# Kernel optimization log

Hardware: AMD Instinct MI355X
Metric: run time of the kernel (lower is better)

## Reference

```python
import jax, jax.numpy as jnp
import numpy as np

NUM_MEM, MEM_DIM, INP_DIM, N = 4096, 512, 1024, 32768

def setup_inputs() -> dict:
    key = jax.random.key(0)
    ks = jax.random.split(key, 6)
    s = 1.0 / np.sqrt(MEM_DIM)
    return {
        "k": jax.random.normal(ks[0], (N, INP_DIM), dtype=jnp.float32),
        "mem": jax.random.normal(ks[1], (NUM_MEM, MEM_DIM), dtype=jnp.float32),
        "fk_w": jax.random.uniform(ks[2], (INP_DIM, MEM_DIM), jnp.float32, -s, s),
        "fk_b": jax.random.uniform(ks[3], (INP_DIM,), jnp.float32, -s, s),
        "fv_w": jax.random.uniform(ks[4], (INP_DIM, MEM_DIM), jnp.float32, -s, s),
        "fv_b": jax.random.uniform(ks[5], (INP_DIM,), jnp.float32, -s, s),
    }

def reference(k, mem, fk_w, fk_b, fv_w, fv_b):
    # key/value derivation from the memory bank: [num_mem, inp_dim]
    key = jax.nn.softmax(mem @ fk_w.T + fk_b, axis=-1)
    val = jax.nn.relu(mem @ fv_w.T + fv_b)
    # attention read: [n, num_mem]
    att = jax.nn.softmax(k @ key.T, axis=-1)
    # output: [n, inp_dim]
    return att @ val
```

## Files before the change

### kernel.cpp

```cpp
#include <hip/hip_runtime.h>
#include <stdint.h>

typedef unsigned short u16;
typedef short s16x8 __attribute__((ext_vector_type(8)));
typedef float f32x4 __attribute__((ext_vector_type(4)));

__device__ __forceinline__ u16 f2bf(float f) {
    union { float f; uint32_t i; } v; v.f = f;
    return (u16)((v.i + 0x7FFFu + ((v.i >> 16) & 1u)) >> 16);
}

__global__ void __launch_bounds__(256) cvt_f32_bf16(
    const float* __restrict__ src, u16* __restrict__ dst, int n4)
{
    int i = blockIdx.x * 256 + threadIdx.x;
    if (i >= n4) return;
    float4 f = ((const float4*)src)[i];
    ushort4 o;
    o.x = f2bf(f.x); o.y = f2bf(f.y); o.z = f2bf(f.z); o.w = f2bf(f.w);
    ((ushort4*)dst)[i] = o;
}

#define ASYNC_LD16(gp, lp)                                                       \
    __builtin_amdgcn_global_load_lds(                                            \
        (const __attribute__((address_space(1))) uint32_t*)(gp),                 \
        (__attribute__((address_space(3))) uint32_t*)(lp), 16, 0, 0)

template <int MODE>
__global__ void __launch_bounds__(256) gemm_bt(
    const u16* __restrict__ A, const u16* __restrict__ B, int K, int N,
    u16* __restrict__ C, float* __restrict__ Cf,
    const float* __restrict__ bias,
    const float* __restrict__ sv, float* __restrict__ sum_out)
{
    __shared__ __align__(16) u16 As[128 * 32];
    __shared__ __align__(16) u16 Bs[128 * 32];

    const int tid  = threadIdx.x;
    const int lane = tid & 63;
    const int wave = tid >> 6;
    const int wx = wave & 1, wy = wave >> 1;
    const int lr = lane & 15, lq = lane >> 4;
    const int m0 = blockIdx.y * 128, n0 = blockIdx.x * 128;

    f32x4 acc[4][4] = {};

    const int srow = tid >> 2;
    const int scol = (tid & 3) * 8;
    const u16* gA = A + (size_t)(m0 + srow) * K + scol;
    const u16* gB = B + (size_t)(n0 + srow) * K + scol;
    const size_t rstep = (size_t)64 * K;
    u16* lA0 = &As[wave * 512];
    u16* lA1 = &As[2048 + wave * 512];
    u16* lB0 = &Bs[wave * 512];
    u16* lB1 = &Bs[2048 + wave * 512];

    const u16* pa = &As[(wy * 64 + lr) * 32 + lq * 8];
    const u16* pb = &Bs[(wx * 64 + lr) * 32 + lq * 8];

    for (int k0 = 0; k0 < K; k0 += 32) {
        ASYNC_LD16(gA + k0, lA0);
        ASYNC_LD16(gA + k0 + rstep, lA1);
        ASYNC_LD16(gB + k0, lB0);
        ASYNC_LD16(gB + k0 + rstep, lB1);
        __syncthreads();
        s16x8 af[4], bfr[4];
#pragma unroll
        for (int i = 0; i < 4; ++i) {
            af[i]  = *(const s16x8*)(pa + i * 512);
            bfr[i] = *(const s16x8*)(pb + i * 512);
        }
#pragma unroll
        for (int mi = 0; mi < 4; ++mi)
#pragma unroll
            for (int ni = 0; ni < 4; ++ni)
                acc[mi][ni] = __builtin_amdgcn_mfma_f32_16x16x32_bf16(
                    af[mi], bfr[ni], acc[mi][ni], 0, 0, 0);
        __syncthreads();
    }

    const int rowB = m0 + wy * 64 + lq * 4;
    const int colB = n0 + wx * 64 + lr;

    if constexpr (MODE == 0) {
        float bcol[4];
#pragma unroll
        for (int ni = 0; ni < 4; ++ni) bcol[ni] = bias[colB + ni * 16];
#pragma unroll
        for (int mi = 0; mi < 4; ++mi)
#pragma unroll
            for (int r = 0; r < 4; ++r) {
                const int gm = rowB + mi * 16 + r;
                float s = 0.f;
#pragma unroll
                for (int ni = 0; ni < 4; ++ni) {
                    float e = __expf(acc[mi][ni][r] + bcol[ni]);
                    C[(size_t)gm * N + (colB + ni * 16)] = f2bf(e);
                    s += e;
                }
                s += __shfl_xor(s, 1);
                s += __shfl_xor(s, 2);
                s += __shfl_xor(s, 4);
                s += __shfl_xor(s, 8);
                if (lr == 0) atomicAdd(&sum_out[gm], s);
            }
    } else {
#pragma unroll
        for (int mi = 0; mi < 4; ++mi)
#pragma unroll
            for (int r = 0; r < 4; ++r) {
                const int gm = rowB + mi * 16 + r;
                const float b = bias[gm];
#pragma unroll
                for (int ni = 0; ni < 4; ++ni) {
                    float c = acc[mi][ni][r] + b;
                    C[(size_t)gm * N + (colB + ni * 16)] = f2bf(c > 0.f ? c : 0.f);
                }
            }
    }
}

template <int MODE>
__global__ void __launch_bounds__(512, 2) gemm256_bt(
    const u16* __restrict__ A, const u16* __restrict__ B, int K, int N,
    u16* __restrict__ C, float* __restrict__ Cf,
    const float* __restrict__ sv, float* __restrict__ sum_out, int nbx)
{
    __shared__ __align__(16) u16 lds[4 * 16384];

    const int tid  = threadIdx.x;
    const int lane = tid & 63;
    const int wave = tid >> 6;
    const int wr = wave >> 2;
    const int wc = wave & 3;
    const int fr = lane & 15;
    const int lq = lane >> 4;

    const int nwg = gridDim.x;
    const int swz = ((int)blockIdx.x & 7) * (nwg >> 3) + ((int)blockIdx.x >> 3);
    const int bx = swz % nbx, by = swz / nbx;
    const int m0 = by * 256, n0 = bx * 256;

    const int r0 = tid >> 2;
    const int r1 = r0 + 128;
    const int gch = (tid & 3) ^ ((r0 >> 1) & 3);
    const u16* gA0 = A + (size_t)(m0 + r0) * K + gch * 8;
    const u16* gA1 = A + (size_t)(m0 + r1) * K + gch * 8;
    const u16* gB0 = B + (size_t)(n0 + r0) * K + gch * 8;
    const u16* gB1 = B + (size_t)(n0 + r1) * K + gch * 8;

#define STG_A(bf_, kt_) do {                                                  \
        ASYNC_LD16(gA0 + (kt_) * 32, lds + (bf_) * 16384 + wave * 512);       \
        ASYNC_LD16(gA1 + (kt_) * 32, lds + (bf_) * 16384 + 4096 + wave * 512);\
    } while (0)
#define STG_B(bf_, kt_) do {                                                  \
        ASYNC_LD16(gB0 + (kt_) * 32, lds + (bf_) * 16384 + 8192 + wave * 512);\
        ASYNC_LD16(gB1 + (kt_) * 32, lds + (bf_) * 16384 + 12288 + wave * 512);\
    } while (0)

    const int rch = lq ^ ((fr >> 1) & 3);
    const int offA0 = (wr * 128 + fr) * 32 + rch * 8;
    const int offB0 = (wc * 64 + fr) * 32 + rch * 8;

    f32x4 acc[8][4] = {};
    const int NT = K >> 5;

    STG_A(0, 0); STG_B(0, 0);
    STG_A(1, 1); STG_B(1, 1);
    STG_A(2, 2); STG_B(2, 2);
    asm volatile("s_waitcnt vmcnt(8)" ::: "memory");
    __builtin_amdgcn_s_barrier();

    for (int c = 0; c < NT; ++c) {
        const u16* sA = lds + (c & 3) * 16384;
        const u16* sB = sA + 8192;
        s16x8 a0[4], b0[4], a1[4];
#pragma unroll
        for (int i = 0; i < 4; ++i) a0[i] = *(const s16x8*)(sA + offA0 + i * 512);
#pragma unroll
        for (int i = 0; i < 4; ++i) b0[i] = *(const s16x8*)(sB + offB0 + i * 512);
        if (c + 3 < NT) STG_A((c + 3) & 3, c + 3);
        __builtin_amdgcn_s_barrier();
        asm volatile("s_waitcnt lgkmcnt(0)" ::: "memory");
        __builtin_amdgcn_s_setprio(1);
#pragma unroll
        for (int mi = 0; mi < 4; ++mi)
#pragma unroll
            for (int ni = 0; ni < 4; ++ni)
                acc[mi][ni] = __builtin_amdgcn_mfma_f32_16x16x32_bf16(
                    a0[mi], b0[ni], acc[mi][ni], 0, 0, 0);
        __builtin_amdgcn_s_setprio(0);
        __builtin_amdgcn_s_barrier();
#pragma unroll
        for (int i = 0; i < 4; ++i) a1[i] = *(const s16x8*)(sA + offA0 + (i + 4) * 512);
        if (c + 3 < NT) STG_B((c + 3) & 3, c + 3);
        __builtin_amdgcn_s_barrier();
        asm volatile("s_waitcnt lgkmcnt(0)" ::: "memory");
        __builtin_amdgcn_s_setprio(1);
#pragma unroll
        for (int mi = 0; mi < 4; ++mi)
#pragma unroll
            for (int ni = 0; ni < 4; ++ni)
                acc[mi + 4][ni] = __builtin_amdgcn_mfma_f32_16x16x32_bf16(
                    a1[mi], b0[ni], acc[mi + 4][ni], 0, 0, 0);
        __builtin_amdgcn_s_setprio(0);
        asm volatile("s_waitcnt vmcnt(8)" ::: "memory");
        __builtin_amdgcn_s_barrier();
    }

    const int rowB = m0 + wr * 128 + lq * 4;
    const int colB = n0 + wc * 64 + fr;

    if constexpr (MODE == 2) {
        float inv[4];
#pragma unroll
        for (int ni = 0; ni < 4; ++ni) inv[ni] = 1.0f / sv[colB + ni * 16];
#pragma unroll
        for (int mi = 0; mi < 8; ++mi)
#pragma unroll
            for (int r = 0; r < 4; ++r) {
                const int gm = rowB + mi * 16 + r;
                float s = 0.f;
#pragma unroll
                for (int ni = 0; ni < 4; ++ni) {
                    float e = __expf(acc[mi][ni][r] * inv[ni]);
                    C[(size_t)gm * N + (colB + ni * 16)] = f2bf(e);
                    s += e;
                }
                s += __shfl_xor(s, 1);
                s += __shfl_xor(s, 2);
                s += __shfl_xor(s, 4);
                s += __shfl_xor(s, 8);
                if (fr == 0) atomicAdd(&sum_out[gm], s);
            }
    } else {
#pragma unroll
        for (int mi = 0; mi < 8; ++mi)
#pragma unroll
            for (int r = 0; r < 4; ++r) {
                const int gm = rowB + mi * 16 + r;
                const float invr = 1.0f / sv[gm];
#pragma unroll
                for (int ni = 0; ni < 4; ++ni)
                    Cf[(size_t)gm * N + (colB + ni * 16)] = acc[mi][ni][r] * invr;
            }
    }
#undef STG_A
#undef STG_B
}

extern "C" void kernel_launch(void* const* d_in, const int* in_sizes, int n_in,
                              void* d_out, int out_size, void* d_ws, size_t ws_size,
                              hipStream_t stream)
{
    (void)in_sizes; (void)n_in; (void)out_size;
    const float* kin = (const float*)d_in[0];
    const float* mem = (const float*)d_in[1];
    const float* fkw = (const float*)d_in[2];
    const float* fkb = (const float*)d_in[3];
    const float* fvw = (const float*)d_in[4];
    const float* fvb = (const float*)d_in[5];
    float* out = (float*)d_out;

    const int NM = 4096, MD = 512, ID = 1024, NQ = 32768;

    u16* kbf   = (u16*)d_ws;
    u16* membf = kbf   + (size_t)NQ * ID;
    u16* fkwbf = membf + (size_t)NM * MD;
    u16* fvwbf = fkwbf + (size_t)ID * MD;
    u16* expK  = fvwbf + (size_t)ID * MD;
    u16* valT  = expK  + (size_t)NM * ID;
    u16* P     = valT  + (size_t)ID * NM;
    float* rsK = (float*)(P + (size_t)NQ * NM);
    float* rs2 = rsK + NM;
    const size_t needed = (size_t)((char*)(rs2 + NQ) - (char*)d_ws);
    if (ws_size < needed) return;

    hipMemsetAsync(rsK, 0, (size_t)(NM + NQ) * sizeof(float), stream);

    cvt_f32_bf16<<<(NQ * ID / 4 + 255) / 256, 256, 0, stream>>>(kin, kbf, NQ * ID / 4);
    cvt_f32_bf16<<<(NM * MD / 4 + 255) / 256, 256, 0, stream>>>(mem, membf, NM * MD / 4);
    cvt_f32_bf16<<<(ID * MD / 4 + 255) / 256, 256, 0, stream>>>(fkw, fkwbf, ID * MD / 4);
    cvt_f32_bf16<<<(ID * MD / 4 + 255) / 256, 256, 0, stream>>>(fvw, fvwbf, ID * MD / 4);

    gemm_bt<0><<<dim3(ID / 128, NM / 128), 256, 0, stream>>>(
        membf, fkwbf, MD, ID, expK, nullptr, fkb, nullptr, rsK);
    gemm_bt<1><<<dim3(NM / 128, ID / 128), 256, 0, stream>>>(
        fvwbf, membf, MD, NM, valT, nullptr, fvb, nullptr, nullptr);
    gemm256_bt<2><<<(NQ / 256) * (NM / 256), 512, 0, stream>>>(
        kbf, expK, ID, NM, P, nullptr, rsK, rs2, NM / 256);
    gemm256_bt<3><<<(NQ / 256) * (ID / 256), 512, 0, stream>>>(
        P, valT, NM, ID, nullptr, out, rs2, nullptr, ID / 256);
}
```

Before: 921.6 us.

## Double K tile to 64 with two-stage LDS double buffering and 8-way swizzle

```diff
diff --git a/kernel.cpp b/kernel.cpp
--- a/kernel.cpp
+++ b/kernel.cpp
@@ -126,7 +126,7 @@
     u16* __restrict__ C, float* __restrict__ Cf,
     const float* __restrict__ sv, float* __restrict__ sum_out, int nbx)
 {
-    __shared__ __align__(16) u16 lds[4 * 16384];
+    __shared__ __align__(16) u16 lds[2 * 32768];
 
     const int tid  = threadIdx.x;
     const int lane = tid & 63;
@@ -141,47 +141,52 @@
     const int bx = swz % nbx, by = swz / nbx;
     const int m0 = by * 256, n0 = bx * 256;
 
-    const int r0 = tid >> 2;
-    const int r1 = r0 + 128;
-    const int gch = (tid & 3) ^ ((r0 >> 1) & 3);
-    const u16* gA0 = A + (size_t)(m0 + r0) * K + gch * 8;
-    const u16* gA1 = A + (size_t)(m0 + r1) * K + gch * 8;
-    const u16* gB0 = B + (size_t)(n0 + r0) * K + gch * 8;
-    const u16* gB1 = B + (size_t)(n0 + r1) * K + gch * 8;
-
-#define STG_A(bf_, kt_) do {                                                  \
-        ASYNC_LD16(gA0 + (kt_) * 32, lds + (bf_) * 16384 + wave * 512);       \
-        ASYNC_LD16(gA1 + (kt_) * 32, lds + (bf_) * 16384 + 4096 + wave * 512);\
+    const int gch = (tid & 7) ^ ((tid >> 4) & 7);
+    const u16* gAb = A + (size_t)(m0 + (tid >> 3)) * K + gch * 8;
+    const u16* gBb = B + (size_t)(n0 + (tid >> 3)) * K + gch * 8;
+    const size_t rst64 = (size_t)64 * K;
+
+#define STG(bf_, kt_) do {                                                    \
+        const u16* _a = gAb + (size_t)(kt_) * 64;                             \
+        const u16* _b = gBb + (size_t)(kt_) * 64;                             \
+        u16* _lA = lds + (bf_) * 32768 + wave * 512;                          \
+        u16* _lB = _lA + 16384;                                               \
+        ASYNC_LD16(_a,             _lA);                                      \
+        ASYNC_LD16(_a + rst64,     _lA + 4096);                               \
+        ASYNC_LD16(_a + 2 * rst64, _lA + 8192);                               \
+        ASYNC_LD16(_a + 3 * rst64, _lA + 12288);                              \
+        ASYNC_LD16(_b,             _lB);                                      \
+        ASYNC_LD16(_b + rst64,     _lB + 4096);                               \
+        ASYNC_LD16(_b + 2 * rst64, _lB + 8192);                               \
+        ASYNC_LD16(_b + 3 * rst64, _lB + 12288);                              \
     } while (0)
-#define STG_B(bf_, kt_) do {                                                  \
-        ASYNC_LD16(gB0 + (kt_) * 32, lds + (bf_) * 16384 + 8192 + wave * 512);\
-        ASYNC_LD16(gB1 + (kt_) * 32, lds + (bf_) * 16384 + 12288 + wave * 512);\
-    } while (0)
-
-    const int rch = lq ^ ((fr >> 1) & 3);
-    const int offA0 = (wr * 128 + fr) * 32 + rch * 8;
-    const int offB0 = (wc * 64 + fr) * 32 + rch * 8;
+
+    const int s7 = (fr >> 1) & 7;
+    const int offAk0 = (wr * 128 + fr) * 64 + ((0 + lq) ^ s7) * 8;
+    const int offAk1 = (wr * 128 + fr) * 64 + ((4 + lq) ^ s7) * 8;
+    const int offBk0 = 16384 + (wc * 64 + fr) * 64 + ((0 + lq) ^ s7) * 8;
+    const int offBk1 = 16384 + (wc * 64 + fr) * 64 + ((4 + lq) ^ s7) * 8;
 
     f32x4 acc[8][4] = {};
-    const int NT = K >> 5;
-
-    STG_A(0, 0); STG_B(0, 0);
-    STG_A(1, 1); STG_B(1, 1);
-    STG_A(2, 2); STG_B(2, 2);
+    const int NT = K >> 6;
+
+    STG(0, 0);
+    STG(1, 1);
     asm volatile("s_waitcnt vmcnt(8)" ::: "memory");
     __builtin_amdgcn_s_barrier();
 
+    s16x8 a0[4], a1[4], b0[4], b1[4];
     for (int c = 0; c < NT; ++c) {
-        const u16* sA = lds + (c & 3) * 16384;
-        const u16* sB = sA + 8192;
-        s16x8 a0[4], b0[4], a1[4];
-#pragma unroll
-        for (int i = 0; i < 4; ++i) a0[i] = *(const s16x8*)(sA + offA0 + i * 512);
-#pragma unroll
-        for (int i = 0; i < 4; ++i) b0[i] = *(const s16x8*)(sB + offB0 + i * 512);
-        if (c + 3 < NT) STG_A((c + 3) & 3, c + 3);
-        __builtin_amdgcn_s_barrier();
-        asm volatile("s_waitcnt lgkmcnt(0)" ::: "memory");
+        const u16* sb = lds + (c & 1) * 32768;
+#pragma unroll
+        for (int i = 0; i < 4; ++i) a0[i] = *(const s16x8*)(sb + offAk0 + i * 1024);
+#pragma unroll
+        for (int i = 0; i < 4; ++i) b0[i] = *(const s16x8*)(sb + offBk0 + i * 1024);
+#pragma unroll
+        for (int i = 0; i < 4; ++i) a1[i] = *(const s16x8*)(sb + offAk1 + i * 1024);
+#pragma unroll
+        for (int i = 0; i < 4; ++i) b1[i] = *(const s16x8*)(sb + offBk1 + i * 1024);
+        __builtin_amdgcn_s_barrier();
         __builtin_amdgcn_s_setprio(1);
 #pragma unroll
         for (int mi = 0; mi < 4; ++mi)
@@ -192,21 +197,47 @@
         __builtin_amdgcn_s_setprio(0);
         __builtin_amdgcn_s_barrier();
 #pragma unroll
-        for (int i = 0; i < 4; ++i) a1[i] = *(const s16x8*)(sA + offA0 + (i + 4) * 512);
-        if (c + 3 < NT) STG_B((c + 3) & 3, c + 3);
-        __builtin_amdgcn_s_barrier();
-        asm volatile("s_waitcnt lgkmcnt(0)" ::: "memory");
+        for (int i = 0; i < 4; ++i) a0[i] = *(const s16x8*)(sb + offAk0 + (i + 4) * 1024);
+        __builtin_amdgcn_s_barrier();
         __builtin_amdgcn_s_setprio(1);
 #pragma unroll
         for (int mi = 0; mi < 4; ++mi)
 #pragma unroll
             for (int ni = 0; ni < 4; ++ni)
+                acc[mi][ni] = __builtin_amdgcn_mfma_f32_16x16x32_bf16(
+                    a1[mi], b1[ni], acc[mi][ni], 0, 0, 0);
+        __builtin_amdgcn_s_setprio(0);
+        __builtin_amdgcn_s_barrier();
+#pragma unroll
+        for (int i = 0; i < 4; ++i) a1[i] = *(const s16x8*)(sb + offAk1 + (i + 4) * 1024);
+        __builtin_amdgcn_s_barrier();
+        __builtin_amdgcn_s_setprio(1);
+#pragma unroll
+        for (int mi = 0; mi < 4; ++mi)
+#pragma unroll
+            for (int ni = 0; ni < 4; ++ni)
                 acc[mi + 4][ni] = __builtin_amdgcn_mfma_f32_16x16x32_bf16(
-                    a1[mi], b0[ni], acc[mi + 4][ni], 0, 0, 0);
+                    a0[mi], b0[ni], acc[mi + 4][ni], 0, 0, 0);
         __builtin_amdgcn_s_setprio(0);
-        asm volatile("s_waitcnt vmcnt(8)" ::: "memory");
+        __builtin_amdgcn_s_barrier();
+        if (c + 2 < NT) {
+            STG(c & 1, c + 2);
+            asm volatile("s_waitcnt vmcnt(8)" ::: "memory");
+        } else {
+            asm volatile("s_waitcnt vmcnt(0)" ::: "memory");
+        }
+        __builtin_amdgcn_s_barrier();
+        __builtin_amdgcn_s_setprio(1);
+#pragma unroll
+        for (int mi = 0; mi < 4; ++mi)
+#pragma unroll
+            for (int ni = 0; ni < 4; ++ni)
+                acc[mi + 4][ni] = __builtin_amdgcn_mfma_f32_16x16x32_bf16(
+                    a1[mi], b1[ni], acc[mi + 4][ni], 0, 0, 0);
+        __builtin_amdgcn_s_setprio(0);
         __builtin_amdgcn_s_barrier();
     }
+#undef STG
 
     const int rowB = m0 + wr * 128 + lq * 4;
     const int colB = n0 + wc * 64 + fr;
@@ -245,8 +276,6 @@
                     Cf[(size_t)gm * N + (colB + ni * 16)] = acc[mi][ni][r] * invr;
             }
     }
-#undef STG_A
-#undef STG_B
 }
 
 extern "C" void kernel_launch(void* const* d_in, const int* in_sizes, int n_in,
```

After: 1.013 ms. +9.9%, slower.
